# Optimization experiments

Hardware: AMD Instinct MI355X
Metric: run time of the kernel (lower is better)

The kernel has to match this reference:

```python
import jax, jax.numpy as jnp
import numpy as np

IN_C = 256
INTER_C = 128


def _conv1x1(x_flat, w, b):
    # x_flat: [n, c_in, N]; w: [c_out, c_in]; b: [c_out] -> [n, c_out, N]
    return jnp.einsum('oc,bcn->bon', w, x_flat) + b[None, :, None]


def setup_inputs() -> dict:
    key = jax.random.key(0)
    ks = jax.random.split(key, 9)
    x = jax.random.normal(ks[0], (4, IN_C, 64, 64), dtype=jnp.float32)
    s_in = 1.0 / np.sqrt(IN_C)
    s_mid = 1.0 / np.sqrt(INTER_C)
    return {
        'x': x,
        'g_w': jax.random.uniform(ks[1], (INTER_C, IN_C), jnp.float32, -s_in, s_in),
        'g_b': jax.random.uniform(ks[2], (INTER_C,), jnp.float32, -s_in, s_in),
        'theta_w': jax.random.uniform(ks[3], (INTER_C, IN_C), jnp.float32, -s_in, s_in),
        'theta_b': jax.random.uniform(ks[4], (INTER_C,), jnp.float32, -s_in, s_in),
        'phi_w': jax.random.uniform(ks[5], (INTER_C, IN_C), jnp.float32, -s_in, s_in),
        'phi_b': jax.random.uniform(ks[6], (INTER_C,), jnp.float32, -s_in, s_in),
        'out_w': jax.random.uniform(ks[7], (IN_C, INTER_C), jnp.float32, -s_mid, s_mid),
        'out_b': jax.random.uniform(ks[8], (IN_C,), jnp.float32, -s_mid, s_mid),
    }


def reference(x, g_w, g_b, theta_w, theta_b, phi_w, phi_b, out_w, out_b):
    n, c, h, w = x.shape
    N = h * w
    x_flat = x.reshape(n, c, N)
    # 1x1-conv projections
    g_x = _conv1x1(x_flat, g_w, g_b).transpose(0, 2, 1)       # [n, N, ci]
    theta_x = _conv1x1(x_flat, theta_w, theta_b).transpose(0, 2, 1)  # [n, N, ci]
    phi_x = _conv1x1(x_flat, phi_w, phi_b)                    # [n, ci, N]
    # dot_product variant: pairwise weight normalized by N (no softmax)
    pairwise_weight = jnp.matmul(theta_x, phi_x) / N          # [n, N, N]
    y = jnp.matmul(pairwise_weight, g_x)                      # [n, N, ci]
    y = y.transpose(0, 2, 1)                                  # [n, ci, N]
    out = x_flat + _conv1x1(y, out_w, out_b)                  # residual
    return out.reshape(n, c, h, w)
```

## Files before the change

### kernel.cpp

```cpp
#include <hip/hip_runtime.h>
#include <hip/hip_bf16.h>


#define CC   256
#define NSP  4096
#define NB   4
#define KSPLIT 16

typedef __attribute__((ext_vector_type(8))) short bf16x8;
typedef __attribute__((ext_vector_type(4))) float f32x4;

#define F_WEND 1048576
#define H_TT   0
#define H_PG   2097152
#define H_S2   6291456
#define H_WH   6356992

__device__ __forceinline__ unsigned short f2bf(float f) {
  __hip_bfloat16 h = __float2bfloat16(f);
  return __builtin_bit_cast(unsigned short, h);
}
__device__ __forceinline__ uint4 pack8(const unsigned short* h) {
  uint4 u;
  u.x = (unsigned)h[0] | ((unsigned)h[1] << 16);
  u.y = (unsigned)h[2] | ((unsigned)h[3] << 16);
  u.z = (unsigned)h[4] | ((unsigned)h[5] << 16);
  u.w = (unsigned)h[6] | ((unsigned)h[7] << 16);
  return u;
}
__device__ __forceinline__ bf16x8 ld_cvt8(const float* __restrict__ p) {
  float4 lo = *(const float4*)p;
  float4 hi = *(const float4*)(p + 4);
  bf16x8 r;
  r[0] = (short)f2bf(lo.x); r[1] = (short)f2bf(lo.y);
  r[2] = (short)f2bf(lo.z); r[3] = (short)f2bf(lo.w);
  r[4] = (short)f2bf(hi.x); r[5] = (short)f2bf(hi.y);
  r[6] = (short)f2bf(hi.z); r[7] = (short)f2bf(hi.w);
  return r;
}

__device__ __forceinline__ void wave_gemm_bt(const unsigned short* __restrict__ A, int pitchA,
                                             const unsigned short* __restrict__ B, int pitchB,
                                             int K, int lane, f32x4 acc[4][4]) {
  int lm = lane & 15, lq = lane >> 4;
  const unsigned short* ap[4];
  const unsigned short* bp[4];
#pragma unroll
  for (int i = 0; i < 4; ++i) {
    ap[i] = A + (size_t)(i * 16 + lm) * pitchA + lq * 8;
    bp[i] = B + (size_t)(i * 16 + lm) * pitchB + lq * 8;
  }
  bf16x8 a0[4], b0[4];
#pragma unroll
  for (int i = 0; i < 4; ++i) {
    a0[i] = *(const bf16x8*)(ap[i]);
    b0[i] = *(const bf16x8*)(bp[i]);
  }
  for (int k = 32; k < K; k += 32) {
    bf16x8 a1[4], b1[4];
#pragma unroll
    for (int i = 0; i < 4; ++i) {
      a1[i] = *(const bf16x8*)(ap[i] + k);
      b1[i] = *(const bf16x8*)(bp[i] + k);
    }
#pragma unroll
    for (int mi = 0; mi < 4; ++mi)
#pragma unroll
      for (int ni = 0; ni < 4; ++ni)
        acc[mi][ni] = __builtin_amdgcn_mfma_f32_16x16x32_bf16(a0[mi], b0[ni], acc[mi][ni], 0, 0, 0);
#pragma unroll
    for (int i = 0; i < 4; ++i) { a0[i] = a1[i]; b0[i] = b1[i]; }
  }
#pragma unroll
  for (int mi = 0; mi < 4; ++mi)
#pragma unroll
    for (int ni = 0; ni < 4; ++ni)
      acc[mi][ni] = __builtin_amdgcn_mfma_f32_16x16x32_bf16(a0[mi], b0[ni], acc[mi][ni], 0, 0, 0);
}

__global__ __launch_bounds__(256) void kW(const float* __restrict__ g_w,
                                          const float* __restrict__ theta_w,
                                          const float* __restrict__ phi_w,
                                          unsigned short* __restrict__ wsh) {
  int idx = (blockIdx.x * 256 + threadIdx.x) * 4;
  int r = idx >> 8;
  const float* src = (r < 128) ? (g_w + idx)
                   : (r < 256) ? (theta_w + idx - 32768)
                               : (phi_w + idx - 65536);
  float4 v = *(const float4*)src;
  uint2 o;
  o.x = (unsigned)f2bf(v.x) | ((unsigned)f2bf(v.y) << 16);
  o.y = (unsigned)f2bf(v.z) | ((unsigned)f2bf(v.w) << 16);
  *(uint2*)(wsh + H_WH + idx) = o;
}

__global__ __launch_bounds__(256) void kP(
    const float* __restrict__ g_b, const float* __restrict__ theta_b,
    const float* __restrict__ phi_b, const float* __restrict__ x,
    unsigned short* __restrict__ wsh) {
  __shared__ float T[64][65];
  __shared__ unsigned short XL[64 * 256];
  __shared__ float biasL[384];
  int bid = blockIdx.x;
  int b = bid >> 6, c = bid & 63;
  int t = threadIdx.x;
  if (t < 128) {
    biasL[t]       = g_b[t];
    biasL[128 + t] = theta_b[t];
    biasL[256 + t] = phi_b[t];
  }
  for (int s = 0; s < 4; ++s) {
    int r = t >> 2, j = t & 3;
    const float* xr = x + ((size_t)b * CC + s * 64 + r) * NSP + c * 64 + j * 16;
    float4 f0 = *(const float4*)(xr);
    float4 f1 = *(const float4*)(xr + 4);
    float4 f2 = *(const float4*)(xr + 8);
    float4 f3 = *(const float4*)(xr + 12);
    *(float4*)&T[r][j * 16 + 0]  = f0;
    *(float4*)&T[r][j * 16 + 4]  = f1;
    *(float4*)&T[r][j * 16 + 8]  = f2;
    *(float4*)&T[r][j * 16 + 12] = f3;
    __syncthreads();
    int nr = t >> 2, j2 = t & 3;
    unsigned short o[16];
#pragma unroll
    for (int i = 0; i < 16; ++i) o[i] = f2bf(T[j2 * 16 + i][nr]);
    int kidx = s * 64 + j2 * 16;
    int sw = (nr & 7) << 3;
    *(uint4*)(XL + ((nr * 256 + kidx) ^ sw))     = pack8(o);
    *(uint4*)(XL + ((nr * 256 + kidx + 8) ^ sw)) = pack8(o + 8);
    __syncthreads();
  }

  int w = t >> 6, lane = t & 63;
  int wm = w >> 1, wn = w & 1;
  int lm = lane & 15, lq = lane >> 4;
  int bsw = (lm & 7) << 3;
  const unsigned short* aw[4];
  int bidx[2];
#pragma unroll
  for (int i = 0; i < 4; ++i)
    aw[i] = wsh + H_WH + (size_t)(wm * 64 + i * 16 + lm) * 256 + lq * 8;
#pragma unroll
  for (int j = 0; j < 2; ++j)
    bidx[j] = (wn * 32 + j * 16 + lm) * 256 + lq * 8;

  f32x4 ag[4][2] = {}, at2[4][2] = {}, ap2[4][2] = {};
#pragma unroll 2
  for (int k = 0; k < 256; k += 32) {
    bf16x8 bb[2], xg[4], xt[4], xp[4];
#pragma unroll
    for (int j = 0; j < 2; ++j) bb[j] = *(const bf16x8*)(XL + ((bidx[j] + k) ^ bsw));
#pragma unroll
    for (int i = 0; i < 4; ++i) {
      xg[i] = *(const bf16x8*)(aw[i] + k);
      xt[i] = *(const bf16x8*)(aw[i] + 32768 + k);
      xp[i] = *(const bf16x8*)(aw[i] + 65536 + k);
    }
#pragma unroll
    for (int mi = 0; mi < 4; ++mi)
#pragma unroll
      for (int ni = 0; ni < 2; ++ni) {
        ag[mi][ni]  = __builtin_amdgcn_mfma_f32_16x16x32_bf16(xg[mi], bb[ni], ag[mi][ni], 0, 0, 0);
        at2[mi][ni] = __builtin_amdgcn_mfma_f32_16x16x32_bf16(xt[mi], bb[ni], at2[mi][ni], 0, 0, 0);
        ap2[mi][ni] = __builtin_amdgcn_mfma_f32_16x16x32_bf16(xp[mi], bb[ni], ap2[mi][ni], 0, 0, 0);
      }
  }

  size_t tb = (size_t)b * 524288;
  size_t pbo = (size_t)b * 1048576;
#pragma unroll
  for (int mi = 0; mi < 4; ++mi) {
    int p0 = wm * 64 + mi * 16 + lq * 4;
#pragma unroll
    for (int ni = 0; ni < 2; ++ni) {
      int n = c * 64 + wn * 32 + ni * 16 + lm;
      unsigned short u0 = f2bf(at2[mi][ni][0] + biasL[128 + p0 + 0]);
      unsigned short u1 = f2bf(at2[mi][ni][1] + biasL[128 + p0 + 1]);
      unsigned short u2 = f2bf(at2[mi][ni][2] + biasL[128 + p0 + 2]);
      unsigned short u3 = f2bf(at2[mi][ni][3] + biasL[128 + p0 + 3]);
      uint2 o;
      o.x = (unsigned)u0 | ((unsigned)u1 << 16);
      o.y = (unsigned)u2 | ((unsigned)u3 << 16);
      *(uint2*)(wsh + H_TT + tb + (size_t)n * 128 + p0) = o;
#pragma unroll
      for (int rr = 0; rr < 4; ++rr) {
        int pl = p0 + rr;
        wsh[H_PG + pbo + (size_t)pl * NSP + n]         = f2bf(ag[mi][ni][rr] + biasL[pl]);
        wsh[H_PG + pbo + (size_t)(128 + pl) * NSP + n] = f2bf(ap2[mi][ni][rr] + biasL[256 + pl]);
      }
    }
  }
}

__global__ __launch_bounds__(256) void kS(const unsigned short* __restrict__ wsh,
                                          float* __restrict__ wsf) {
  int bid = blockIdx.x;
  int b = bid >> 4, ks = bid & 15;
  int t = threadIdx.x, w = t >> 6, lane = t & 63;
  int lm = lane & 15, lq = lane >> 4;
  int qm = w >> 1, qn = w & 1;
  const unsigned short* A = wsh + H_PG + (size_t)b * 1048576 +
                            (size_t)(128 + qm * 64) * NSP + ks * 256;
  const unsigned short* B = wsh + H_PG + (size_t)b * 1048576 +
                            (size_t)(qn * 64) * NSP + ks * 256;
  f32x4 acc[4][4] = {};
  wave_gemm_bt(A, NSP, B, NSP, 256, lane, acc);
  float* P = wsf + (size_t)(b * KSPLIT + ks) * 16384;
#pragma unroll
  for (int mi = 0; mi < 4; ++mi)
#pragma unroll
    for (int rr = 0; rr < 4; ++rr) {
      int p = qm * 64 + mi * 16 + lq * 4 + rr;
#pragma unroll
      for (int ni = 0; ni < 4; ++ni)
        P[p * 128 + qn * 64 + ni * 16 + lm] = acc[mi][ni][rr];
    }
}

__global__ __launch_bounds__(256) void kR(const float* __restrict__ wsf,
                                          unsigned short* __restrict__ wsh) {
  int bid = blockIdx.x;
  int b = bid >> 4, e = bid & 15;
  int t = threadIdx.x;
  int base = e * 1024 + t * 4;
  const float* PB = wsf + (size_t)b * KSPLIT * 16384;
  float4 s = {0.f, 0.f, 0.f, 0.f};
#pragma unroll
  for (int ks = 0; ks < KSPLIT; ++ks) {
    float4 p = *(const float4*)(PB + (size_t)ks * 16384 + base);
    s.x += p.x; s.y += p.y; s.z += p.z; s.w += p.w;
  }
  uint2 o;
  o.x = (unsigned)f2bf(s.x) | ((unsigned)f2bf(s.y) << 16);
  o.y = (unsigned)f2bf(s.z) | ((unsigned)f2bf(s.w) << 16);
  *(uint2*)(wsh + H_S2 + (size_t)b * 16384 + base) = o;
}

__global__ __launch_bounds__(256) void kD(const unsigned short* __restrict__ wsh,
                                          const float* __restrict__ out_w,
                                          const float* __restrict__ x,
                                          const float* __restrict__ out_b,
                                          float* __restrict__ out) {
  __shared__ unsigned short W2L[128 * 128];
  int bid = blockIdx.x;
  int b = bid >> 6, r6 = bid & 63;
  int tm = r6 >> 5, tn = r6 & 31;
  int t = threadIdx.x, w = t >> 6, lane = t & 63;
  int lm = lane & 15, lq = lane >> 4;
  int rb = tm * 128;

  {
    int pm = w >> 1, im = w & 1;
    const unsigned short* As = wsh + H_S2 + (size_t)b * 16384;
    f32x4 macc[4][4] = {};
    for (int kk = 0; kk < 128; kk += 32) {
      bf16x8 a[4], bb[4];
#pragma unroll
      for (int i = 0; i < 4; ++i) {
        a[i]  = *(const bf16x8*)(As + (size_t)(pm * 64 + i * 16 + lm) * 128 + lq * 8 + kk);
        bb[i] = ld_cvt8(out_w + (size_t)(rb + im * 64 + i * 16 + lm) * 128 + lq * 8 + kk);
      }
#pragma unroll
      for (int mi = 0; mi < 4; ++mi)
#pragma unroll
        for (int ni = 0; ni < 4; ++ni)
          macc[mi][ni] = __builtin_amdgcn_mfma_f32_16x16x32_bf16(a[mi], bb[ni], macc[mi][ni], 0, 0, 0);
    }
    const float inv = 1.0f / 4096.0f;
#pragma unroll
    for (int mi = 0; mi < 4; ++mi) {
      int p0 = pm * 64 + mi * 16 + lq * 4;
#pragma unroll
      for (int ni = 0; ni < 4; ++ni) {
        int il = im * 64 + ni * 16 + lm;
        unsigned short u0 = f2bf(macc[mi][ni][0] * inv);
        unsigned short u1 = f2bf(macc[mi][ni][1] * inv);
        unsigned short u2 = f2bf(macc[mi][ni][2] * inv);
        unsigned short u3 = f2bf(macc[mi][ni][3] * inv);
        uint2 o;
        o.x = (unsigned)u0 | ((unsigned)u1 << 16);
        o.y = (unsigned)u2 | ((unsigned)u3 << 16);
        *(uint2*)(W2L + ((il * 128 + p0) ^ ((il & 7) << 3))) = o;
      }
    }
  }
  __syncthreads();

  int wm = w >> 1, wn = w & 1;
  int cb = tn * 128 + wn * 64;
  int asw = (lm & 7) << 3;
  int aidx[4];
  const unsigned short* bp[4];
#pragma unroll
  for (int i = 0; i < 4; ++i) {
    aidx[i] = (wm * 64 + i * 16 + lm) * 128 + lq * 8;
    bp[i] = wsh + H_TT + (size_t)b * 524288 + (size_t)(cb + i * 16 + lm) * 128 + lq * 8;
  }
  f32x4 acc[4][4] = {};
  bf16x8 a0[4], b0[4];
#pragma unroll
  for (int i = 0; i < 4; ++i) {
    a0[i] = *(const bf16x8*)(W2L + (aidx[i] ^ asw));
    b0[i] = *(const bf16x8*)(bp[i]);
  }
  for (int k = 32; k < 128; k += 32) {
    bf16x8 a1[4], b1[4];
#pragma unroll
    for (int i = 0; i < 4; ++i) {
      a1[i] = *(const bf16x8*)(W2L + ((aidx[i] + k) ^ asw));
      b1[i] = *(const bf16x8*)(bp[i] + k);
    }
#pragma unroll
    for (int mi = 0; mi < 4; ++mi)
#pragma unroll
      for (int ni = 0; ni < 4; ++ni)
        acc[mi][ni] = __builtin_amdgcn_mfma_f32_16x16x32_bf16(a0[mi], b0[ni], acc[mi][ni], 0, 0, 0);
#pragma unroll
    for (int i = 0; i < 4; ++i) { a0[i] = a1[i]; b0[i] = b1[i]; }
  }
#pragma unroll
  for (int mi = 0; mi < 4; ++mi)
#pragma unroll
    for (int ni = 0; ni < 4; ++ni)
      acc[mi][ni] = __builtin_amdgcn_mfma_f32_16x16x32_bf16(a0[mi], b0[ni], acc[mi][ni], 0, 0, 0);

#pragma unroll
  for (int mi = 0; mi < 4; ++mi)
#pragma unroll
    for (int rr = 0; rr < 4; ++rr) {
      int row = rb + wm * 64 + mi * 16 + lq * 4 + rr;
      float bi = out_b[row];
#pragma unroll
      for (int ni = 0; ni < 4; ++ni) {
        int col = cb + ni * 16 + lm;
        size_t off = ((size_t)b * CC + row) * NSP + col;
        out[off] = acc[mi][ni][rr] + x[off] + bi;
      }
    }
}

extern "C" void kernel_launch(void* const* d_in, const int* in_sizes, int n_in,
                              void* d_out, int out_size, void* d_ws, size_t ws_size,
                              hipStream_t stream) {
  const float* x       = (const float*)d_in[0];
  const float* g_w     = (const float*)d_in[1];
  const float* g_b     = (const float*)d_in[2];
  const float* theta_w = (const float*)d_in[3];
  const float* theta_b = (const float*)d_in[4];
  const float* phi_w   = (const float*)d_in[5];
  const float* phi_b   = (const float*)d_in[6];
  const float* out_w   = (const float*)d_in[7];
  const float* out_b   = (const float*)d_in[8];
  float* wsf = (float*)d_ws;
  unsigned short* wsh = (unsigned short*)(wsf + F_WEND);
  float* out = (float*)d_out;

  kW<<<dim3(96), dim3(256), 0, stream>>>(g_w, theta_w, phi_w, wsh);
  kP<<<dim3(256), dim3(256), 0, stream>>>(g_b, theta_b, phi_b, x, wsh);
  kS<<<dim3(64), dim3(256), 0, stream>>>(wsh, wsf);
  kR<<<dim3(64), dim3(256), 0, stream>>>(wsf, wsh);
  kD<<<dim3(256), dim3(256), 0, stream>>>(wsh, out_w, x, out_b, out);
}
```

Measured before the change: 126.4 us.

## Hoist out_w×S2 product into separate kernel and double grid sizes for kP/kD

Pre-converts out_w to bf16 in kW, and moves the per-block recomputation of W2 = out_w·S2/N out of kD into a new small kernel kW2 that computes it once per batch. kP and kD now use half-size tiles so each launches 512 blocks instead of 256, giving more parallelism across CUs. kP also stages its g/phi outputs through shared memory so they can be written to global as coalesced 16-byte rows instead of scattered 2-byte stores. In exchange there is an extra kernel launch and a W2 round trip through global memory, and the smaller tiles reuse less data per block.

```diff
diff --git a/kernel.cpp b/kernel.cpp
--- a/kernel.cpp
+++ b/kernel.cpp
@@ -15,6 +15,8 @@
 #define H_PG   2097152
 #define H_S2   6291456
 #define H_WH   6356992
+#define H_OWH  6455296
+#define H_W2   6488064
 
 __device__ __forceinline__ unsigned short f2bf(float f) {
   __hip_bfloat16 h = __float2bfloat16(f);
@@ -28,16 +30,6 @@
   u.w = (unsigned)h[6] | ((unsigned)h[7] << 16);
   return u;
 }
-__device__ __forceinline__ bf16x8 ld_cvt8(const float* __restrict__ p) {
-  float4 lo = *(const float4*)p;
-  float4 hi = *(const float4*)(p + 4);
-  bf16x8 r;
-  r[0] = (short)f2bf(lo.x); r[1] = (short)f2bf(lo.y);
-  r[2] = (short)f2bf(lo.z); r[3] = (short)f2bf(lo.w);
-  r[4] = (short)f2bf(hi.x); r[5] = (short)f2bf(hi.y);
-  r[6] = (short)f2bf(hi.z); r[7] = (short)f2bf(hi.w);
-  return r;
-}
 
 __device__ __forceinline__ void wave_gemm_bt(const unsigned short* __restrict__ A, int pitchA,
                                              const unsigned short* __restrict__ B, int pitchB,
@@ -81,28 +73,37 @@
 __global__ __launch_bounds__(256) void kW(const float* __restrict__ g_w,
                                           const float* __restrict__ theta_w,
                                           const float* __restrict__ phi_w,
+                                          const float* __restrict__ out_w,
                                           unsigned short* __restrict__ wsh) {
   int idx = (blockIdx.x * 256 + threadIdx.x) * 4;
-  int r = idx >> 8;
-  const float* src = (r < 128) ? (g_w + idx)
-                   : (r < 256) ? (theta_w + idx - 32768)
-                               : (phi_w + idx - 65536);
+  const float* src;
+  unsigned short* dst;
+  if (idx < 98304) {
+    int r = idx >> 8;
+    src = (r < 128) ? (g_w + idx)
+        : (r < 256) ? (theta_w + idx - 32768)
+                    : (phi_w + idx - 65536);
+    dst = wsh + H_WH + idx;
+  } else {
+    src = out_w + (idx - 98304);
+    dst = wsh + H_OWH + (idx - 98304);
+  }
   float4 v = *(const float4*)src;
   uint2 o;
   o.x = (unsigned)f2bf(v.x) | ((unsigned)f2bf(v.y) << 16);
   o.y = (unsigned)f2bf(v.z) | ((unsigned)f2bf(v.w) << 16);
-  *(uint2*)(wsh + H_WH + idx) = o;
+  *(uint2*)dst = o;
 }
 
 __global__ __launch_bounds__(256) void kP(
     const float* __restrict__ g_b, const float* __restrict__ theta_b,
     const float* __restrict__ phi_b, const float* __restrict__ x,
     unsigned short* __restrict__ wsh) {
-  __shared__ float T[64][65];
-  __shared__ unsigned short XL[64 * 256];
+  __shared__ float T[64][33];
+  __shared__ unsigned short XL[32 * 256];
   __shared__ float biasL[384];
   int bid = blockIdx.x;
-  int b = bid >> 6, c = bid & 63;
+  int b = bid >> 7, c = bid & 127;
   int t = threadIdx.x;
   if (t < 128) {
     biasL[t]       = g_b[t];
@@ -111,54 +112,50 @@
   }
   for (int s = 0; s < 4; ++s) {
     int r = t >> 2, j = t & 3;
-    const float* xr = x + ((size_t)b * CC + s * 64 + r) * NSP + c * 64 + j * 16;
+    const float* xr = x + ((size_t)b * CC + s * 64 + r) * NSP + c * 32 + j * 8;
     float4 f0 = *(const float4*)(xr);
     float4 f1 = *(const float4*)(xr + 4);
-    float4 f2 = *(const float4*)(xr + 8);
-    float4 f3 = *(const float4*)(xr + 12);
-    *(float4*)&T[r][j * 16 + 0]  = f0;
-    *(float4*)&T[r][j * 16 + 4]  = f1;
-    *(float4*)&T[r][j * 16 + 8]  = f2;
-    *(float4*)&T[r][j * 16 + 12] = f3;
+    T[r][j * 8 + 0] = f0.x; T[r][j * 8 + 1] = f0.y;
+    T[r][j * 8 + 2] = f0.z; T[r][j * 8 + 3] = f0.w;
+    T[r][j * 8 + 4] = f1.x; T[r][j * 8 + 5] = f1.y;
+    T[r][j * 8 + 6] = f1.z; T[r][j * 8 + 7] = f1.w;
     __syncthreads();
-    int nr = t >> 2, j2 = t & 3;
-    unsigned short o[16];
-#pragma unroll
-    for (int i = 0; i < 16; ++i) o[i] = f2bf(T[j2 * 16 + i][nr]);
-    int kidx = s * 64 + j2 * 16;
+    int nr = t >> 3, j2 = t & 7;
+    unsigned short o[8];
+#pragma unroll
+    for (int i = 0; i < 8; ++i) o[i] = f2bf(T[j2 * 8 + i][nr]);
+    int kidx = s * 64 + j2 * 8;
     int sw = (nr & 7) << 3;
-    *(uint4*)(XL + ((nr * 256 + kidx) ^ sw))     = pack8(o);
-    *(uint4*)(XL + ((nr * 256 + kidx + 8) ^ sw)) = pack8(o + 8);
+    *(uint4*)(XL + ((nr * 256 + kidx) ^ sw)) = pack8(o);
     __syncthreads();
   }
 
   int w = t >> 6, lane = t & 63;
-  int wm = w >> 1, wn = w & 1;
   int lm = lane & 15, lq = lane >> 4;
   int bsw = (lm & 7) << 3;
-  const unsigned short* aw[4];
+  const unsigned short* aw[2];
   int bidx[2];
 #pragma unroll
-  for (int i = 0; i < 4; ++i)
-    aw[i] = wsh + H_WH + (size_t)(wm * 64 + i * 16 + lm) * 256 + lq * 8;
+  for (int i = 0; i < 2; ++i)
+    aw[i] = wsh + H_WH + (size_t)(w * 32 + i * 16 + lm) * 256 + lq * 8;
 #pragma unroll
   for (int j = 0; j < 2; ++j)
-    bidx[j] = (wn * 32 + j * 16 + lm) * 256 + lq * 8;
-
-  f32x4 ag[4][2] = {}, at2[4][2] = {}, ap2[4][2] = {};
+    bidx[j] = (j * 16 + lm) * 256 + lq * 8;
+
+  f32x4 ag[2][2] = {}, at2[2][2] = {}, ap2[2][2] = {};
 #pragma unroll 2
   for (int k = 0; k < 256; k += 32) {
-    bf16x8 bb[2], xg[4], xt[4], xp[4];
+    bf16x8 bb[2], xg[2], xt[2], xp[2];
 #pragma unroll
     for (int j = 0; j < 2; ++j) bb[j] = *(const bf16x8*)(XL + ((bidx[j] + k) ^ bsw));
 #pragma unroll
-    for (int i = 0; i < 4; ++i) {
+    for (int i = 0; i < 2; ++i) {
       xg[i] = *(const bf16x8*)(aw[i] + k);
       xt[i] = *(const bf16x8*)(aw[i] + 32768 + k);
       xp[i] = *(const bf16x8*)(aw[i] + 65536 + k);
     }
 #pragma unroll
-    for (int mi = 0; mi < 4; ++mi)
+    for (int mi = 0; mi < 2; ++mi)
 #pragma unroll
       for (int ni = 0; ni < 2; ++ni) {
         ag[mi][ni]  = __builtin_amdgcn_mfma_f32_16x16x32_bf16(xg[mi], bb[ni], ag[mi][ni], 0, 0, 0);
@@ -168,13 +165,12 @@
   }
 
   size_t tb = (size_t)b * 524288;
-  size_t pbo = (size_t)b * 1048576;
-#pragma unroll
-  for (int mi = 0; mi < 4; ++mi) {
-    int p0 = wm * 64 + mi * 16 + lq * 4;
+#pragma unroll
+  for (int mi = 0; mi < 2; ++mi) {
+    int p0 = w * 32 + mi * 16 + lq * 4;
 #pragma unroll
     for (int ni = 0; ni < 2; ++ni) {
-      int n = c * 64 + wn * 32 + ni * 16 + lm;
+      int n = c * 32 + ni * 16 + lm;
       unsigned short u0 = f2bf(at2[mi][ni][0] + biasL[128 + p0 + 0]);
       unsigned short u1 = f2bf(at2[mi][ni][1] + biasL[128 + p0 + 1]);
       unsigned short u2 = f2bf(at2[mi][ni][2] + biasL[128 + p0 + 2]);
@@ -183,13 +179,30 @@
       o.x = (unsigned)u0 | ((unsigned)u1 << 16);
       o.y = (unsigned)u2 | ((unsigned)u3 << 16);
       *(uint2*)(wsh + H_TT + tb + (size_t)n * 128 + p0) = o;
+    }
+  }
+
+  __syncthreads();
+#pragma unroll
+  for (int mi = 0; mi < 2; ++mi)
+#pragma unroll
+    for (int ni = 0; ni < 2; ++ni) {
+      int nl = ni * 16 + lm;
 #pragma unroll
       for (int rr = 0; rr < 4; ++rr) {
-        int pl = p0 + rr;
-        wsh[H_PG + pbo + (size_t)pl * NSP + n]         = f2bf(ag[mi][ni][rr] + biasL[pl]);
-        wsh[H_PG + pbo + (size_t)(128 + pl) * NSP + n] = f2bf(ap2[mi][ni][rr] + biasL[256 + pl]);
+        int p = w * 32 + mi * 16 + lq * 4 + rr;
+        XL[p * 32 + nl]         = f2bf(ag[mi][ni][rr] + biasL[p]);
+        XL[(128 + p) * 32 + nl] = f2bf(ap2[mi][ni][rr] + biasL[256 + p]);
       }
     }
+  __syncthreads();
+  size_t pbo = (size_t)b * 1048576;
+#pragma unroll
+  for (int r4 = 0; r4 < 4; ++r4) {
+    int row = r4 * 64 + (t >> 2);
+    int coff = (t & 3) * 8;
+    *(uint4*)(wsh + H_PG + pbo + (size_t)row * NSP + c * 32 + coff) =
+        *(uint4*)(XL + row * 32 + coff);
   }
 }
 
@@ -237,102 +250,100 @@
   *(uint2*)(wsh + H_S2 + (size_t)b * 16384 + base) = o;
 }
 
+__global__ __launch_bounds__(256) void kW2(unsigned short* __restrict__ wsh) {
+  int bid = blockIdx.x;
+  int b = bid >> 2, is = bid & 3;
+  int t = threadIdx.x, w = t >> 6, lane = t & 63;
+  int lm = lane & 15, lq = lane >> 4;
+  const unsigned short* A = wsh + H_OWH + (size_t)(is * 64) * 128;
+  const unsigned short* B = wsh + H_S2 + (size_t)b * 16384 + (size_t)(w * 32) * 128;
+  f32x4 acc[4][2] = {};
+  for (int k = 0; k < 128; k += 32) {
+    bf16x8 a[4], bb[2];
+#pragma unroll
+    for (int i = 0; i < 4; ++i)
+      a[i] = *(const bf16x8*)(A + (size_t)(i * 16 + lm) * 128 + lq * 8 + k);
+#pragma unroll
+    for (int j = 0; j < 2; ++j)
+      bb[j] = *(const bf16x8*)(B + (size_t)(j * 16 + lm) * 128 + lq * 8 + k);
+#pragma unroll
+    for (int mi = 0; mi < 4; ++mi)
+#pragma unroll
+      for (int ni = 0; ni < 2; ++ni)
+        acc[mi][ni] = __builtin_amdgcn_mfma_f32_16x16x32_bf16(a[mi], bb[ni], acc[mi][ni], 0, 0, 0);
+  }
+  const float inv = 1.0f / 4096.0f;
+#pragma unroll
+  for (int mi = 0; mi < 4; ++mi)
+#pragma unroll
+    for (int rr = 0; rr < 4; ++rr) {
+      int i = is * 64 + mi * 16 + lq * 4 + rr;
+#pragma unroll
+      for (int ni = 0; ni < 2; ++ni) {
+        int p = w * 32 + ni * 16 + lm;
+        wsh[H_W2 + (size_t)b * 32768 + (size_t)i * 128 + p] = f2bf(acc[mi][ni][rr] * inv);
+      }
+    }
+}
+
 __global__ __launch_bounds__(256) void kD(const unsigned short* __restrict__ wsh,
-                                          const float* __restrict__ out_w,
                                           const float* __restrict__ x,
                                           const float* __restrict__ out_b,
                                           float* __restrict__ out) {
-  __shared__ unsigned short W2L[128 * 128];
-  int bid = blockIdx.x;
-  int b = bid >> 6, r6 = bid & 63;
-  int tm = r6 >> 5, tn = r6 & 31;
+  int bid = blockIdx.x;
+  int b = bid >> 7, r7 = bid & 127;
+  int tm = r7 >> 6, tn = r7 & 63;
   int t = threadIdx.x, w = t >> 6, lane = t & 63;
-  int lm = lane & 15, lq = lane >> 4;
-  int rb = tm * 128;
-
-  {
-    int pm = w >> 1, im = w & 1;
-    const unsigned short* As = wsh + H_S2 + (size_t)b * 16384;
-    f32x4 macc[4][4] = {};
-    for (int kk = 0; kk < 128; kk += 32) {
-      bf16x8 a[4], bb[4];
-#pragma unroll
-      for (int i = 0; i < 4; ++i) {
-        a[i]  = *(const bf16x8*)(As + (size_t)(pm * 64 + i * 16 + lm) * 128 + lq * 8 + kk);
-        bb[i] = ld_cvt8(out_w + (size_t)(rb + im * 64 + i * 16 + lm) * 128 + lq * 8 + kk);
-      }
-#pragma unroll
-      for (int mi = 0; mi < 4; ++mi)
-#pragma unroll
-        for (int ni = 0; ni < 4; ++ni)
-          macc[mi][ni] = __builtin_amdgcn_mfma_f32_16x16x32_bf16(a[mi], bb[ni], macc[mi][ni], 0, 0, 0);
-    }
-    const float inv = 1.0f / 4096.0f;
-#pragma unroll
-    for (int mi = 0; mi < 4; ++mi) {
-      int p0 = pm * 64 + mi * 16 + lq * 4;
-#pragma unroll
-      for (int ni = 0; ni < 4; ++ni) {
-        int il = im * 64 + ni * 16 + lm;
-        unsigned short u0 = f2bf(macc[mi][ni][0] * inv);
-        unsigned short u1 = f2bf(macc[mi][ni][1] * inv);
-        unsigned short u2 = f2bf(macc[mi][ni][2] * inv);
-        unsigned short u3 = f2bf(macc[mi][ni][3] * inv);
-        uint2 o;
-        o.x = (unsigned)u0 | ((unsigned)u1 << 16);
-        o.y = (unsigned)u2 | ((unsigned)u3 << 16);
-        *(uint2*)(W2L + ((il * 128 + p0) ^ ((il & 7) << 3))) = o;
-      }
-    }
-  }
-  __syncthreads();
-
   int wm = w >> 1, wn = w & 1;
-  int cb = tn * 128 + wn * 64;
-  int asw = (lm & 7) << 3;
-  int aidx[4];
-  const unsigned short* bp[4];
-#pragma unroll
-  for (int i = 0; i < 4; ++i) {
-    aidx[i] = (wm * 64 + i * 16 + lm) * 128 + lq * 8;
-    bp[i] = wsh + H_TT + (size_t)b * 524288 + (size_t)(cb + i * 16 + lm) * 128 + lq * 8;
-  }
-  f32x4 acc[4][4] = {};
-  bf16x8 a0[4], b0[4];
-#pragma unroll
-  for (int i = 0; i < 4; ++i) {
-    a0[i] = *(const bf16x8*)(W2L + (aidx[i] ^ asw));
-    b0[i] = *(const bf16x8*)(bp[i]);
-  }
+  int lm = lane & 15, lq = lane >> 4;
+  int rb = tm * 128 + wm * 64, cb = tn * 64 + wn * 32;
+  const unsigned short* A = wsh + H_W2 + (size_t)b * 32768;
+  const unsigned short* B = wsh + H_TT + (size_t)b * 524288;
+  const unsigned short* ap[4];
+  const unsigned short* bp[2];
+#pragma unroll
+  for (int i = 0; i < 4; ++i)
+    ap[i] = A + (size_t)(rb + i * 16 + lm) * 128 + lq * 8;
+#pragma unroll
+  for (int j = 0; j < 2; ++j)
+    bp[j] = B + (size_t)(cb + j * 16 + lm) * 128 + lq * 8;
+
+  f32x4 acc[4][2] = {};
+  bf16x8 a0[4], b0[2];
+#pragma unroll
+  for (int i = 0; i < 4; ++i) a0[i] = *(const bf16x8*)(ap[i]);
+#pragma unroll
+  for (int j = 0; j < 2; ++j) b0[j] = *(const bf16x8*)(bp[j]);
   for (int k = 32; k < 128; k += 32) {
-    bf16x8 a1[4], b1[4];
-#pragma unroll
-    for (int i = 0; i < 4; ++i) {
-      a1[i] = *(const bf16x8*)(W2L + ((aidx[i] + k) ^ asw));
-      b1[i] = *(const bf16x8*)(bp[i] + k);
-    }
+    bf16x8 a1[4], b1[2];
+#pragma unroll
+    for (int i = 0; i < 4; ++i) a1[i] = *(const bf16x8*)(ap[i] + k);
+#pragma unroll
+    for (int j = 0; j < 2; ++j) b1[j] = *(const bf16x8*)(bp[j] + k);
 #pragma unroll
     for (int mi = 0; mi < 4; ++mi)
 #pragma unroll
-      for (int ni = 0; ni < 4; ++ni)
+      for (int ni = 0; ni < 2; ++ni)
         acc[mi][ni] = __builtin_amdgcn_mfma_f32_16x16x32_bf16(a0[mi], b0[ni], acc[mi][ni], 0, 0, 0);
 #pragma unroll
-    for (int i = 0; i < 4; ++i) { a0[i] = a1[i]; b0[i] = b1[i]; }
-  }
-#pragma unroll
-  for (int mi = 0; mi < 4; ++mi)
-#pragma unroll
-    for (int ni = 0; ni < 4; ++ni)
+    for (int i = 0; i < 4; ++i) a0[i] = a1[i];
+#pragma unroll
+    for (int j = 0; j < 2; ++j) b0[j] = b1[j];
+  }
+#pragma unroll
+  for (int mi = 0; mi < 4; ++mi)
+#pragma unroll
+    for (int ni = 0; ni < 2; ++ni)
       acc[mi][ni] = __builtin_amdgcn_mfma_f32_16x16x32_bf16(a0[mi], b0[ni], acc[mi][ni], 0, 0, 0);
 
 #pragma unroll
   for (int mi = 0; mi < 4; ++mi)
 #pragma unroll
     for (int rr = 0; rr < 4; ++rr) {
-      int row = rb + wm * 64 + mi * 16 + lq * 4 + rr;
+      int row = rb + mi * 16 + lq * 4 + rr;
       float bi = out_b[row];
 #pragma unroll
-      for (int ni = 0; ni < 4; ++ni) {
+      for (int ni = 0; ni < 2; ++ni) {
         int col = cb + ni * 16 + lm;
         size_t off = ((size_t)b * CC + row) * NSP + col;
         out[off] = acc[mi][ni][rr] + x[off] + bi;
@@ -356,9 +367,10 @@
   unsigned short* wsh = (unsigned short*)(wsf + F_WEND);
   float* out = (float*)d_out;
 
-  kW<<<dim3(96), dim3(256), 0, stream>>>(g_w, theta_w, phi_w, wsh);
-  kP<<<dim3(256), dim3(256), 0, stream>>>(g_b, theta_b, phi_b, x, wsh);
+  kW<<<dim3(128), dim3(256), 0, stream>>>(g_w, theta_w, phi_w, out_w, wsh);
+  kP<<<dim3(512), dim3(256), 0, stream>>>(g_b, theta_b, phi_b, x, wsh);
   kS<<<dim3(64), dim3(256), 0, stream>>>(wsh, wsf);
   kR<<<dim3(64), dim3(256), 0, stream>>>(wsf, wsh);
-  kD<<<dim3(256), dim3(256), 0, stream>>>(wsh, out_w, x, out_b, out);
-}
+  kW2<<<dim3(16), dim3(256), 0, stream>>>(wsh);
+  kD<<<dim3(512), dim3(256), 0, stream>>>(wsh, x, out_b, out);
+}
```

After: 125.8 us (median of 2 runs). About the same (-0.5%).
